# Optimization experiments

Hardware: AMD Instinct MI355X
Metric: run time of the kernel (lower is better)

The kernel has to match this reference:

```python
import jax, jax.numpy as jnp
import numpy as np

B, L, V, D, H, DK, NL, M = 4, 1024, 64, 256, 4, 64, 4, 20
FF = 4 * D
EPS = 1e-5


def _rel_table(seq_len, m):
    # abs(i-j), log-bucketed beyond m, clipped to [0, 2m] -> int indices [L, L]
    d = jnp.abs(jnp.arange(seq_len)[:, None] - jnp.arange(seq_len)[None, :]).astype(jnp.float32)
    d = jnp.where(d > m, m + jnp.log2(jnp.maximum(d - m, 1.0)), d)
    return jnp.clip(d, 0, 2 * m).astype(jnp.int32)


def _layer_norm(x, g, b):
    mu = jnp.mean(x, axis=-1, keepdims=True)
    var = jnp.mean(jnp.square(x - mu), axis=-1, keepdims=True)
    return (x - mu) * jax.lax.rsqrt(var + EPS) * g + b


def setup_inputs() -> dict:
    key = jax.random.key(0)
    ks = jax.random.split(key, 16)
    w = lambda i, shape: jax.random.normal(ks[i], shape, jnp.float32) * 0.05
    return {
        "x": jax.random.normal(ks[0], (B, L, V), jnp.float32),
        "emb": w(1, (V, D)),
        "Wq": w(2, (NL, D, H * DK)), "bq": jnp.zeros((NL, H * DK), jnp.float32),
        "Wk": w(3, (NL, D, H * DK)), "bk": jnp.zeros((NL, H * DK), jnp.float32),
        "Wv": w(4, (NL, D, H * DK)), "bv": jnp.zeros((NL, H * DK), jnp.float32),
        "Wo": w(5, (NL, H * DK, D)), "bo": jnp.zeros((NL, D), jnp.float32),
        "rel_k": 1.0 + w(6, (NL, 2 * M + 1, H)),  # multiplicative bias ~1
        "rel_b": w(7, (NL, 2 * M + 1, H)),
        "ln1_g": jnp.ones((NL, D), jnp.float32), "ln1_b": jnp.zeros((NL, D), jnp.float32),
        "W1": w(8, (NL, D, FF)), "b1": jnp.zeros((NL, FF), jnp.float32),
        "W2": w(9, (NL, FF, D)), "b2": jnp.zeros((NL, D), jnp.float32),
        "ln2_g": jnp.ones((NL, D), jnp.float32), "ln2_b": jnp.zeros((NL, D), jnp.float32),
    }


def reference(x, emb, Wq, bq, Wk, bk, Wv, bv, Wo, bo, rel_k, rel_b,
              ln1_g, ln1_b, W1, b1, W2, b2, ln2_g, ln2_b):
    h = x @ emb  # [B, L, D]  (dropout inactive: eval mode)
    table = _rel_table(L, M)  # [L, L] int32
    inv_sqrt_dk = jnp.float32(1.0 / np.sqrt(DK))
    attns = []
    for l in range(NL):
        q = (h @ Wq[l] + bq[l]).reshape(B, L, H, DK)
        k = (h @ Wk[l] + bk[l]).reshape(B, L, H, DK)
        v = (h @ Wv[l] + bv[l]).reshape(B, L, H, DK)
        scores = jnp.einsum('blhk,bmhk->bhlm', q, k) * inv_sqrt_dk
        # per-head relative-position bias (table symmetric, so axis order of L,L is immaterial)
        bias_k = jnp.transpose(rel_k[l][table], (2, 1, 0))  # [H, L, L]
        bias_b = jnp.transpose(rel_b[l][table], (2, 1, 0))  # [H, L, L]
        scores = scores * bias_k[None] + bias_b[None]
        attn = jax.nn.softmax(scores, axis=-1)  # attn dropout inactive (eval)
        attns.append(attn)
        out = jnp.einsum('bhlm,bmhk->blhk', attn, v).reshape(B, L, H * DK) @ Wo[l] + bo[l]
        # FeedForwardNetwork (note: source has NO residual connections)
        y = _layer_norm(out, ln1_g[l], ln1_b[l])
        y = jax.nn.gelu(y @ W1[l] + b1[l], approximate=False) @ W2[l] + b2[l]
        h = _layer_norm(y, ln2_g[l], ln2_b[l])
    avg_attn = jnp.mean(jnp.stack(attns, axis=0), axis=0)  # [B, H, L, L]
    return h.mean(axis=1), avg_attn
```

## Files before the change

### kernel.cpp

```cpp
#include <hip/hip_runtime.h>
#include <hip/hip_bf16.h>
#include <math.h>

#define Bn 4
#define Ln 1024
#define Vn 64
#define Dn 256
#define Hn 4
#define DKn 64
#define NLn 4
#define Mn 20
#define FFn 1024
#define NTOK (Bn * Ln)
#define QKVW 768
#define LOG2E 1.4426950408889634f
#define PELEMS (Bn * Hn * Ln * Ln)

typedef __attribute__((ext_vector_type(8))) short bf16x8;
typedef __attribute__((ext_vector_type(4))) float f32x4;

__device__ __forceinline__ ushort f2b(float f) {
    uint u = __float_as_uint(f);
    u += 0x7fff + ((u >> 16) & 1);
    return (ushort)(u >> 16);
}
__device__ __forceinline__ float b2f(ushort u) {
    return __uint_as_float(((uint)u) << 16);
}

__global__ __launch_bounds__(256) void embed_k(const float* __restrict__ X,
                                               const float* __restrict__ E,
                                               ushort* __restrict__ Hb) {
    __shared__ float xs[Vn];
    int n = blockIdx.x, d = threadIdx.x;
    if (threadIdx.x < Vn) xs[threadIdx.x] = X[n * Vn + threadIdx.x];
    __syncthreads();
    float s = 0.f;
#pragma unroll
    for (int v = 0; v < Vn; ++v) s += xs[v] * E[v * Dn + d];
    Hb[(size_t)n * Dn + d] = f2b(s);
}

__global__ __launch_bounds__(256) void relbias_k(const float* __restrict__ rk,
                                                 const float* __restrict__ rb,
                                                 float* __restrict__ bkT,
                                                 float* __restrict__ bbT) {
    int tid = blockIdx.x * 256 + threadIdx.x;
    int dist = tid & 1023;
    int hh = (tid >> 10) & 3;
    int l = tid >> 12;
    float dd = (float)dist;
    if (dist > Mn) dd = (float)Mn + log2f((float)(dist - Mn));
    if (dd > 2.0f * Mn) dd = 2.0f * Mn;
    int idx = (int)dd;
    bkT[tid] = rk[(l * (2 * Mn + 1) + idx) * Hn + hh] * 0.125f * LOG2E;
    bbT[tid] = rb[(l * (2 * Mn + 1) + idx) * Hn + hh] * LOG2E;
}

__global__ __launch_bounds__(256) void prep_bias(const float* __restrict__ bq,
                                                 const float* __restrict__ bk,
                                                 const float* __restrict__ bv,
                                                 float* __restrict__ bqkv) {
    int idx = blockIdx.x * 256 + threadIdx.x;
    int l = idx / QKVW, r = idx - l * QKVW;
    float v;
    if (r < 256)      v = bq[l * 256 + r];
    else if (r < 512) v = bk[l * 256 + r - 256];
    else              v = bv[l * 256 + r - 512];
    bqkv[idx] = v;
}

__global__ __launch_bounds__(256) void transpose_cvt(
    const float* __restrict__ src, ushort* __restrict__ dst,
    int R, int C, int srcLS, int dstLS) {
    __shared__ float s[32][33];
    src += (size_t)blockIdx.z * srcLS;
    dst += (size_t)blockIdx.z * dstLS;
    int r0 = blockIdx.y * 32, c0 = blockIdx.x * 32;
    int tx = threadIdx.x & 31, ty = threadIdx.x >> 5;
#pragma unroll
    for (int ii = 0; ii < 4; ++ii)
        s[ty + 8 * ii][tx] = src[(size_t)(r0 + ty + 8 * ii) * C + c0 + tx];
    __syncthreads();
#pragma unroll
    for (int ii = 0; ii < 4; ++ii)
        dst[(size_t)(c0 + ty + 8 * ii) * R + r0 + tx] = f2b(s[tx][ty + 8 * ii]);
}

#define GST 72
#define GEMM_KK_MFMA(KK)                                                      \
    {                                                                         \
        bf16x8 a0 = *(const bf16x8*)&As[(wm * 32 + l15) * GST + (KK)*32 + lg * 8];      \
        bf16x8 a1 = *(const bf16x8*)&As[(wm * 32 + 16 + l15) * GST + (KK)*32 + lg * 8]; \
        bf16x8 b0 = *(const bf16x8*)&Bs[(wn * 32 + l15) * GST + (KK)*32 + lg * 8];      \
        bf16x8 b1 = *(const bf16x8*)&Bs[(wn * 32 + 16 + l15) * GST + (KK)*32 + lg * 8]; \
        acc[0][0] = __builtin_amdgcn_mfma_f32_16x16x32_bf16(a0, b0, acc[0][0], 0, 0, 0); \
        acc[0][1] = __builtin_amdgcn_mfma_f32_16x16x32_bf16(a0, b1, acc[0][1], 0, 0, 0); \
        acc[1][0] = __builtin_amdgcn_mfma_f32_16x16x32_bf16(a1, b0, acc[1][0], 0, 0, 0); \
        acc[1][1] = __builtin_amdgcn_mfma_f32_16x16x32_bf16(a1, b1, acc[1][1], 0, 0, 0); \
    }

template <int LNA>
__global__ __launch_bounds__(256) void gemm_mfma(
    const ushort* __restrict__ A, const ushort* __restrict__ Bt,
    const float* __restrict__ bias, ushort* __restrict__ C,
    int M, int N, int K, int act,
    const float* __restrict__ lng, const float* __restrict__ lnb,
    ushort* __restrict__ Vt_out) {
    __shared__ __align__(16) ushort As[64 * GST];
    __shared__ __align__(16) ushort Bs[64 * GST];
    __shared__ float gl[256];
    __shared__ float bl[256];
    int t = threadIdx.x;
    int lane = t & 63, w = t >> 6;
    int wm = w >> 1, wn = w & 1;
    int l15 = lane & 15, lg = lane >> 4;
    int mBase = blockIdx.y * 64, nBase = blockIdx.x * 64;
    int lrow = t >> 2, lkc = (t & 3) * 16;
    const ushort* Ap = A + (size_t)(mBase + lrow) * K + lkc;
    const ushort* Bp = Bt + (size_t)(nBase + lrow) * K + lkc;
    f32x4 acc[2][2] = {};

    if constexpr (LNA) {
        uint4 areg[8];
        float s = 0.f;
#pragma unroll
        for (int kc = 0; kc < 4; ++kc)
#pragma unroll
            for (int h = 0; h < 2; ++h) {
                areg[kc * 2 + h] = *(const uint4*)(Ap + kc * 64 + h * 8);
                const ushort* e = (const ushort*)&areg[kc * 2 + h];
#pragma unroll
                for (int q = 0; q < 8; ++q) s += b2f(e[q]);
            }
        s += __shfl_xor(s, 1, 64);
        s += __shfl_xor(s, 2, 64);
        float mu = s * (1.0f / 256.0f);
        float vv = 0.f;
#pragma unroll
        for (int kc = 0; kc < 8; ++kc) {
            const ushort* e = (const ushort*)&areg[kc];
#pragma unroll
            for (int q = 0; q < 8; ++q) {
                float d = b2f(e[q]) - mu;
                vv += d * d;
            }
        }
        vv += __shfl_xor(vv, 1, 64);
        vv += __shfl_xor(vv, 2, 64);
        float rs = rsqrtf(vv * (1.0f / 256.0f) + 1e-5f);
        gl[t] = lng[t];
        bl[t] = lnb[t];
        __syncthreads();
#pragma unroll
        for (int kc = 0; kc < 4; ++kc) {
            uint4 bv0 = *(const uint4*)(Bp + kc * 64);
            uint4 bv1 = *(const uint4*)(Bp + kc * 64 + 8);
            __syncthreads();
#pragma unroll
            for (int h = 0; h < 2; ++h) {
                const ushort* e = (const ushort*)&areg[kc * 2 + h];
                ushort outv[8];
#pragma unroll
                for (int q = 0; q < 8; ++q) {
                    int col = kc * 64 + lkc + h * 8 + q;
                    outv[q] = f2b((b2f(e[q]) - mu) * rs * gl[col] + bl[col]);
                }
                *(uint4*)&As[lrow * GST + lkc + h * 8] = *(const uint4*)outv;
            }
            *(uint4*)&Bs[lrow * GST + lkc] = bv0;
            *(uint4*)&Bs[lrow * GST + lkc + 8] = bv1;
            __syncthreads();
            GEMM_KK_MFMA(0)
            GEMM_KK_MFMA(1)
        }
    } else {
        for (int k0 = 0; k0 < K; k0 += 64) {
            uint4 av0 = *(const uint4*)(Ap + k0);
            uint4 av1 = *(const uint4*)(Ap + k0 + 8);
            uint4 bv0 = *(const uint4*)(Bp + k0);
            uint4 bv1 = *(const uint4*)(Bp + k0 + 8);
            __syncthreads();
            *(uint4*)&As[lrow * GST + lkc] = av0;
            *(uint4*)&As[lrow * GST + lkc + 8] = av1;
            *(uint4*)&Bs[lrow * GST + lkc] = bv0;
            *(uint4*)&Bs[lrow * GST + lkc + 8] = bv1;
            __syncthreads();
            GEMM_KK_MFMA(0)
            GEMM_KK_MFMA(1)
        }
    }
    if (Vt_out != nullptr && nBase >= 512) {
#pragma unroll
        for (int ni = 0; ni < 2; ++ni) {
            int col = nBase + wn * 32 + ni * 16 + l15;
            float bc = bias[col];
            int d = col - 512;
#pragma unroll
            for (int mi = 0; mi < 2; ++mi) {
                int rb = mBase + wm * 32 + mi * 16 + lg * 4;
                int bb_ = rb >> 10, i_ = rb & 1023;
                size_t vb = ((size_t)(bb_ * 4 + (d >> 6)) * 64 + (d & 63)) * Ln + i_;
                ushort o4[4];
#pragma unroll
                for (int j = 0; j < 4; ++j) o4[j] = f2b(acc[mi][ni][j] + bc);
                *(ushort4*)&Vt_out[vb] = *(const ushort4*)o4;
            }
        }
        return;
    }
#pragma unroll
    for (int ni = 0; ni < 2; ++ni) {
        int col = nBase + wn * 32 + ni * 16 + l15;
        float bc = bias[col];
#pragma unroll
        for (int mi = 0; mi < 2; ++mi) {
            int rb = mBase + wm * 32 + mi * 16 + lg * 4;
#pragma unroll
            for (int j = 0; j < 4; ++j) {
                float v = acc[mi][ni][j] + bc;
                if (act) v = v * 0.5f * (1.0f + erff(v * 0.7071067811865475f));
                C[(size_t)(rb + j) * N + col] = f2b(v);
            }
        }
    }
}

#define PWST 40
#define NW 8
template <int MODE>
__global__ __launch_bounds__(512) void attn_fused(
    const ushort* __restrict__ qkv, const ushort* __restrict__ Vt,
    const float* __restrict__ bkTab, const float* __restrict__ bbTab,
    ushort* __restrict__ ctx, float* __restrict__ avg,
    ushort* __restrict__ Pout, int first) {
    __shared__ float bk_l[Ln];
    __shared__ float bb_l[Ln];
    __shared__ __align__(16) char uni[20480];
    __shared__ float mm[NW][16];
    __shared__ float ll[NW][16];

    int t = threadIdx.x;
    int lane = t & 63, w = t >> 6;
    int wn = w & 3, wc = w >> 2;
    int l15 = lane & 15, lg = lane >> 4;

    ushort* pwh = (ushort*)&uni[w * 2560];
    ushort* pwl = (ushort*)&uni[w * 2560 + 1280];

    int bid = blockIdx.x;
    int xcd = bid & 7, sub = bid >> 3;
    int bh = xcd * 2 + (sub >> 6);
    int q = sub & 63;
    int b = bh >> 2, hh = bh & 3;
    int i0 = q * 16;

#pragma unroll
    for (int ii = 0; ii < 2; ++ii) {
        bk_l[t + 512 * ii] = bkTab[hh * Ln + t + 512 * ii];
        bb_l[t + 512 * ii] = bbTab[hh * Ln + t + 512 * ii];
    }
    __syncthreads();

    bf16x8 qa0, qa1;
    {
        const ushort* qp = qkv + (size_t)(b * Ln + i0 + l15) * QKVW + hh * DKn;
        qa0 = *(const bf16x8*)(qp + lg * 8);
        qa1 = *(const bf16x8*)(qp + 32 + lg * 8);
    }

    const ushort* kbase = qkv + (size_t)(b * Ln) * QKVW + Dn + hh * DKn;

    f32x4 sv[8];
    float m[4] = {-1e30f, -1e30f, -1e30f, -1e30f};
#pragma unroll
    for (int cl = 0; cl < 8; ++cl) {
        int c = wc * 8 + cl;
        const ushort* kp = kbase + (size_t)(c * 64 + wn * 16 + l15) * QKVW;
        bf16x8 k0 = *(const bf16x8*)(kp + lg * 8);
        bf16x8 k1 = *(const bf16x8*)(kp + 32 + lg * 8);
        f32x4 acc = {};
        acc = __builtin_amdgcn_mfma_f32_16x16x32_bf16(qa0, k0, acc, 0, 0, 0);
        acc = __builtin_amdgcn_mfma_f32_16x16x32_bf16(qa1, k1, acc, 0, 0, 0);
        int j = c * 64 + wn * 16 + l15;
#pragma unroll
        for (int r = 0; r < 4; ++r) {
            int i = i0 + lg * 4 + r;
            int dist = (i > j) ? (i - j) : (j - i);
            float s = acc[r] * bk_l[dist] + bb_l[dist];
            sv[cl][r] = s;
            m[r] = fmaxf(m[r], s);
        }
    }
#pragma unroll
    for (int mask = 1; mask < 16; mask <<= 1)
#pragma unroll
        for (int r = 0; r < 4; ++r) m[r] = fmaxf(m[r], __shfl_xor(m[r], mask, 64));
    if (l15 == 0)
#pragma unroll
        for (int r = 0; r < 4; ++r) mm[w][lg * 4 + r] = m[r];
    __syncthreads();
#pragma unroll
    for (int r = 0; r < 4; ++r) {
        int row = lg * 4 + r;
        float m0 = fmaxf(fmaxf(mm[0][row], mm[1][row]), fmaxf(mm[2][row], mm[3][row]));
        float m1 = fmaxf(fmaxf(mm[4][row], mm[5][row]), fmaxf(mm[6][row], mm[7][row]));
        m[r] = fmaxf(m0, m1);
    }
    float lsum[4] = {0.f, 0.f, 0.f, 0.f};
#pragma unroll
    for (int cl = 0; cl < 8; ++cl)
#pragma unroll
        for (int r = 0; r < 4; ++r) {
            float p = exp2f(sv[cl][r] - m[r]);
            sv[cl][r] = p;
            lsum[r] += p;
        }
#pragma unroll
    for (int mask = 1; mask < 16; mask <<= 1)
#pragma unroll
        for (int r = 0; r < 4; ++r) lsum[r] += __shfl_xor(lsum[r], mask, 64);
    if (l15 == 0)
#pragma unroll
        for (int r = 0; r < 4; ++r) ll[w][lg * 4 + r] = lsum[r];
    __syncthreads();
    float invl[4];
#pragma unroll
    for (int r = 0; r < 4; ++r) {
        int row = lg * 4 + r;
        invl[r] = 1.0f / (ll[0][row] + ll[1][row] + ll[2][row] + ll[3][row] +
                          ll[4][row] + ll[5][row] + ll[6][row] + ll[7][row]);
    }

    const ushort* vbase = Vt + (size_t)bh * DKn * Ln;
    float* avgrow = avg + ((size_t)bh * Ln + i0) * Ln;
    int iw = lane >> 2, jq = lane & 3;
    f32x4 acco[4] = {};
#pragma unroll
    for (int p = 0; p < 4; ++p) {
        const int c0 = wc * 8 + 2 * p, c1 = c0 + 1;
        float aold[2][4];
        if (MODE == 0 && !first) {
#pragma unroll
            for (int cc = 0; cc < 2; ++cc)
#pragma unroll
                for (int r = 0; r < 4; ++r)
                    aold[cc][r] = avgrow[(size_t)(lg * 4 + r) * Ln +
                                         (c0 + cc) * 64 + wn * 16 + l15];
        }
#pragma unroll
        for (int cc = 0; cc < 2; ++cc)
#pragma unroll
            for (int r = 0; r < 4; ++r) {
                float pv = sv[2 * p + cc][r] * invl[r];
                sv[2 * p + cc][r] = pv;
                ushort ph = f2b(pv);
                int off = (lg * 4 + r) * PWST + cc * 16 + l15;
                pwh[off] = ph;
                pwl[off] = f2b(pv - b2f(ph));
            }
        int kcol = (lg < 2 ? c0 : c1) * 64 + wn * 16 + (lg & 1) * 8;
        bf16x8 va0 = *(const bf16x8*)(vbase + (size_t)(0 * 16 + l15) * Ln + kcol);
        bf16x8 va1 = *(const bf16x8*)(vbase + (size_t)(1 * 16 + l15) * Ln + kcol);
        bf16x8 va2 = *(const bf16x8*)(vbase + (size_t)(2 * 16 + l15) * Ln + kcol);
        bf16x8 va3 = *(const bf16x8*)(vbase + (size_t)(3 * 16 + l15) * Ln + kcol);
        bf16x8 pbh = *(const bf16x8*)&pwh[l15 * PWST + lg * 8];
        bf16x8 pbl = *(const bf16x8*)&pwl[l15 * PWST + lg * 8];
        acco[0] = __builtin_amdgcn_mfma_f32_16x16x32_bf16(va0, pbh, acco[0], 0, 0, 0);
        acco[1] = __builtin_amdgcn_mfma_f32_16x16x32_bf16(va1, pbh, acco[1], 0, 0, 0);
        acco[2] = __builtin_amdgcn_mfma_f32_16x16x32_bf16(va2, pbh, acco[2], 0, 0, 0);
        acco[3] = __builtin_amdgcn_mfma_f32_16x16x32_bf16(va3, pbh, acco[3], 0, 0, 0);
        acco[0] = __builtin_amdgcn_mfma_f32_16x16x32_bf16(va0, pbl, acco[0], 0, 0, 0);
        acco[1] = __builtin_amdgcn_mfma_f32_16x16x32_bf16(va1, pbl, acco[1], 0, 0, 0);
        acco[2] = __builtin_amdgcn_mfma_f32_16x16x32_bf16(va2, pbl, acco[2], 0, 0, 0);
        acco[3] = __builtin_amdgcn_mfma_f32_16x16x32_bf16(va3, pbl, acco[3], 0, 0, 0);
        if (MODE == 0) {
#pragma unroll
            for (int cc = 0; cc < 2; ++cc)
#pragma unroll
                for (int r = 0; r < 4; ++r) {
                    float v = 0.25f * sv[2 * p + cc][r];
                    if (!first) v += aold[cc][r];
                    avgrow[(size_t)(lg * 4 + r) * Ln + (c0 + cc) * 64 + wn * 16 + l15] = v;
                }
        } else if (MODE == 1) {
            size_t tb = ((((size_t)bid * 8 + w) * 4 + p) * 2) * 256 + (size_t)lane * 4;
            ushort4 ph0 = *(const ushort4*)&pwh[iw * PWST + 0 * 16 + jq * 4];
            ushort4 ph1 = *(const ushort4*)&pwh[iw * PWST + 1 * 16 + jq * 4];
            *(ushort4*)&Pout[tb] = ph0;
            *(ushort4*)&Pout[tb + 256] = ph1;
        } else {
#pragma unroll
            for (int cc = 0; cc < 2; ++cc) {
                int c = c0 + cc;
                size_t tb = ((((size_t)bid * 8 + w) * 4 + p) * 2 + cc) * 256 +
                            (size_t)lane * 4;
                ushort4 p0 = *(const ushort4*)&Pout[tb];
                ushort4 p1 = *(const ushort4*)&Pout[(size_t)PELEMS + tb];
                ushort4 p2 = *(const ushort4*)&Pout[(size_t)2 * PELEMS + tb];
                ushort4 p3 = *(const ushort4*)&pwh[iw * PWST + cc * 16 + jq * 4];
                const ushort* q0 = (const ushort*)&p0;
                const ushort* q1 = (const ushort*)&p1;
                const ushort* q2 = (const ushort*)&p2;
                const ushort* q3 = (const ushort*)&p3;
                size_t base = ((size_t)(bh * Ln) + i0 + iw) * Ln +
                              c * 64 + wn * 16 + jq * 4;
                float4 o;
                float* op_ = (float*)&o;
#pragma unroll
                for (int k = 0; k < 4; ++k)
                    op_[k] = 0.25f * (b2f(q0[k]) + b2f(q1[k]) + b2f(q2[k]) + b2f(q3[k]));
                *(float4*)&avg[base] = o;
            }
        }
    }

    __syncthreads();
    {
        float* op = (float*)&uni[wn * 4096];
        if (wc == 1) {
#pragma unroll
            for (int dg = 0; dg < 4; ++dg)
#pragma unroll
                for (int r = 0; r < 4; ++r)
                    op[(dg * 16 + lg * 4 + r) * 16 + l15] = acco[dg][r];
        }
    }
    __syncthreads();
    {
        float* op = (float*)&uni[wn * 4096];
        if (wc == 0) {
#pragma unroll
            for (int dg = 0; dg < 4; ++dg)
#pragma unroll
                for (int r = 0; r < 4; ++r)
                    op[(dg * 16 + lg * 4 + r) * 16 + l15] += acco[dg][r];
        }
    }
    __syncthreads();
#pragma unroll
    for (int k = 0; k < 2; ++k) {
        int idx = t + 512 * k;
        float v = ((const float*)&uni[0])[idx] + ((const float*)&uni[4096])[idx] +
                  ((const float*)&uni[8192])[idx] + ((const float*)&uni[12288])[idx];
        int dd = idx >> 4, ii = idx & 15;
        ctx[(size_t)(b * Ln + i0 + ii) * Dn + hh * DKn + dd] = f2b(v);
    }
}

__global__ __launch_bounds__(256) void layernorm_k(const ushort* __restrict__ X,
                                                   const float* __restrict__ g,
                                                   const float* __restrict__ bta,
                                                   ushort* __restrict__ Y) {
    int w = threadIdx.x >> 6, lane = threadIdx.x & 63;
    int row = blockIdx.x * 4 + w;
    const ushort* xr = X + (size_t)row * Dn;
    float x[4];
#pragma unroll
    for (int ii = 0; ii < 4; ++ii) x[ii] = b2f(xr[lane + 64 * ii]);
    float s = x[0] + x[1] + x[2] + x[3];
#pragma unroll
    for (int m = 1; m < 64; m <<= 1) s += __shfl_xor(s, m, 64);
    float mu = s * (1.0f / 256.0f);
    float vs = 0.f;
#pragma unroll
    for (int ii = 0; ii < 4; ++ii) {
        float d = x[ii] - mu;
        vs += d * d;
    }
#pragma unroll
    for (int m = 1; m < 64; m <<= 1) vs += __shfl_xor(vs, m, 64);
    float rs = rsqrtf(vs * (1.0f / 256.0f) + 1e-5f);
#pragma unroll
    for (int ii = 0; ii < 4; ++ii) {
        int d = lane + 64 * ii;
        Y[(size_t)row * Dn + d] = f2b((x[ii] - mu) * rs * g[d] + bta[d]);
    }
}

__global__ __launch_bounds__(256) void mean_part_k(const ushort* __restrict__ Hb,
                                                   float* __restrict__ part) {
    int blk = blockIdx.x;
    int b = blk >> 4, g = blk & 15;
    int d = threadIdx.x;
    float s = 0.f;
#pragma unroll
    for (int r = 0; r < 64; ++r)
        s += b2f(Hb[(size_t)(b * Ln + g * 64 + r) * Dn + d]);
    part[(size_t)blk * Dn + d] = s;
}
__global__ __launch_bounds__(256) void mean_final_k(const float* __restrict__ part,
                                                    float* __restrict__ out) {
    int b = blockIdx.x, d = threadIdx.x;
    float s = 0.f;
#pragma unroll
    for (int g = 0; g < 16; ++g) s += part[(size_t)(b * 16 + g) * Dn + d];
    out[b * Dn + d] = s * (1.0f / (float)Ln);
}

extern "C" void kernel_launch(void* const* d_in, const int* in_sizes, int n_in,
                              void* d_out, int out_size, void* d_ws, size_t ws_size,
                              hipStream_t stream) {
    const float* x    = (const float*)d_in[0];
    const float* emb  = (const float*)d_in[1];
    const float* Wq   = (const float*)d_in[2];
    const float* bq   = (const float*)d_in[3];
    const float* Wk   = (const float*)d_in[4];
    const float* bk   = (const float*)d_in[5];
    const float* Wv   = (const float*)d_in[6];
    const float* bv   = (const float*)d_in[7];
    const float* Wo   = (const float*)d_in[8];
    const float* bo   = (const float*)d_in[9];
    const float* rk   = (const float*)d_in[10];
    const float* rb   = (const float*)d_in[11];
    const float* ln1g = (const float*)d_in[12];
    const float* ln1b = (const float*)d_in[13];
    const float* W1   = (const float*)d_in[14];
    const float* b1   = (const float*)d_in[15];
    const float* W2   = (const float*)d_in[16];
    const float* b2   = (const float*)d_in[17];
    const float* ln2g = (const float*)d_in[18];
    const float* ln2b = (const float*)d_in[19];

    float* out = (float*)d_out;
    float* avg = out + Bn * Dn;

    char* ws = (char*)d_ws;
    const size_t MB = 1024 * 1024;
    ushort* hb   = (ushort*)(ws);
    ushort* qkvb = (ushort*)(ws + 2 * MB);
    ushort* ctxb = (ushort*)(ws + 8 * MB);
    ushort* t1   = (ushort*)(ws + 10 * MB);
    ushort* ffb  = (ushort*)(ws + 12 * MB);
    ushort* qkvT = (ushort*)(ws + 20 * MB);
    ushort* WoT  = (ushort*)(ws + 22 * MB);
    ushort* W1T  = (ushort*)(ws + 23 * MB);
    ushort* W2T  = (ushort*)(ws + 25 * MB);
    float*  bqkv = (float*)(ws + 27 * MB);
    float*  bkT  = (float*)(ws + 27 * MB + 65536);
    float*  bbT  = (float*)(ws + 27 * MB + 131072);
    ushort* Vt   = (ushort*)(ws + 30 * MB);
    float*  mpart= (float*)(ws + 33 * MB);
    ushort* Pbuf = (ushort*)(ws + 36 * MB);

    const size_t need = 36 * MB + (size_t)3 * PELEMS * sizeof(ushort);
    const bool fancy = (ws_size >= need);

    embed_k<<<NTOK, 256, 0, stream>>>(x, emb, hb);
    relbias_k<<<64, 256, 0, stream>>>(rk, rb, bkT, bbT);
    prep_bias<<<12, 256, 0, stream>>>(bq, bk, bv, bqkv);

    dim3 t88(8, 8, NLn);
    transpose_cvt<<<t88, 256, 0, stream>>>(Wq, qkvT + 0,      256, 256, 65536, 196608);
    transpose_cvt<<<t88, 256, 0, stream>>>(Wk, qkvT + 65536,  256, 256, 65536, 196608);
    transpose_cvt<<<t88, 256, 0, stream>>>(Wv, qkvT + 131072, 256, 256, 65536, 196608);
    transpose_cvt<<<t88, 256, 0, stream>>>(Wo, WoT,           256, 256, 65536, 65536);
    transpose_cvt<<<dim3(32, 8, NLn), 256, 0, stream>>>(W1, W1T, 256, 1024, 262144, 262144);
    transpose_cvt<<<dim3(8, 32, NLn), 256, 0, stream>>>(W2, W2T, 1024, 256, 262144, 262144);

    for (int l = 0; l < NLn; ++l) {
        if (l == 0) {
            gemm_mfma<0><<<dim3(12, 64), 256, 0, stream>>>(
                hb, qkvT + (size_t)l * 196608, bqkv + l * QKVW, qkvb,
                NTOK, QKVW, Dn, 0, nullptr, nullptr, Vt);
        } else {
            gemm_mfma<1><<<dim3(12, 64), 256, 0, stream>>>(
                hb, qkvT + (size_t)l * 196608, bqkv + l * QKVW, qkvb,
                NTOK, QKVW, Dn, 0, ln2g + (l - 1) * 256, ln2b + (l - 1) * 256, Vt);
        }
        if (fancy) {
            if (l < 3) {
                attn_fused<1><<<1024, 512, 0, stream>>>(
                    qkvb, Vt, bkT + l * Hn * Ln, bbT + l * Hn * Ln, ctxb, avg,
                    Pbuf + (size_t)l * PELEMS, 0);
            } else {
                attn_fused<2><<<1024, 512, 0, stream>>>(
                    qkvb, Vt, bkT + l * Hn * Ln, bbT + l * Hn * Ln, ctxb, avg,
                    Pbuf, 0);
            }
        } else {
            attn_fused<0><<<1024, 512, 0, stream>>>(
                qkvb, Vt, bkT + l * Hn * Ln, bbT + l * Hn * Ln, ctxb, avg,
                (ushort*)Pbuf, (l == 0) ? 1 : 0);
        }
        gemm_mfma<0><<<dim3(4, 64), 256, 0, stream>>>(
            ctxb, WoT + (size_t)l * 65536, bo + l * 256, t1,
            NTOK, Dn, Dn, 0, nullptr, nullptr, nullptr);
        gemm_mfma<1><<<dim3(16, 64), 256, 0, stream>>>(
            t1, W1T + (size_t)l * 262144, b1 + l * FFn, ffb,
            NTOK, FFn, Dn, 1, ln1g + l * 256, ln1b + l * 256, nullptr);
        gemm_mfma<0><<<dim3(4, 64), 256, 0, stream>>>(
            ffb, W2T + (size_t)l * 262144, b2 + l * 256, hb,
            NTOK, Dn, FFn, 0, nullptr, nullptr, nullptr);
    }
    layernorm_k<<<NTOK / 4, 256, 0, stream>>>(
        hb, ln2g + 3 * 256, ln2b + 3 * 256, hb);
    mean_part_k<<<64, 256, 0, stream>>>(hb, mpart);
    mean_final_k<<<Bn, 256, 0, stream>>>(mpart, out);
}
```

Baseline: 375.5 us.

## Add 128x128-tile MFMA GEMM with fused LayerNorm and split-K FFN down-projection

```diff
diff --git a/kernel.cpp b/kernel.cpp
--- a/kernel.cpp
+++ b/kernel.cpp
@@ -224,6 +224,177 @@
             }
         }
     }
+}
+
+#define G2ST 72
+template <int LNA, int SPLITK>
+__global__ __launch_bounds__(256) void gemm128(
+    const ushort* __restrict__ A, const ushort* __restrict__ Bt,
+    const float* __restrict__ bias, ushort* __restrict__ C,
+    float* __restrict__ Cpart,
+    int M, int N, int K, int act,
+    const float* __restrict__ lng, const float* __restrict__ lnb,
+    ushort* __restrict__ Vt_out) {
+    __shared__ __align__(16) ushort As[128 * G2ST];
+    __shared__ __align__(16) ushort Bs[128 * G2ST];
+    __shared__ float gl[256];
+    __shared__ float bl[256];
+    int t = threadIdx.x;
+    int lane = t & 63, w = t >> 6;
+    int wm = w >> 1, wn = w & 1;
+    int l15 = lane & 15, lg = lane >> 4;
+    int mBase = blockIdx.y * 128, nBase = blockIdx.x * 128;
+    int srow = t >> 1, skof = (t & 1) * 32;
+    int kchunk = (SPLITK > 1) ? (K / SPLITK) : K;
+    int kbeg = (SPLITK > 1) ? blockIdx.z * kchunk : 0;
+    const ushort* Ap = A + (size_t)(mBase + srow) * K + kbeg + skof;
+    const ushort* Bp = Bt + (size_t)(nBase + srow) * K + kbeg + skof;
+    f32x4 acc[4][4] = {};
+
+    float mu = 0.f, rs = 0.f;
+    uint4 areg[16];
+    if constexpr (LNA) {
+        float s = 0.f;
+#pragma unroll
+        for (int kc = 0; kc < 4; ++kc)
+#pragma unroll
+            for (int q = 0; q < 4; ++q) {
+                areg[kc * 4 + q] = *(const uint4*)(Ap + kc * 64 + q * 8);
+                const ushort* e = (const ushort*)&areg[kc * 4 + q];
+#pragma unroll
+                for (int z = 0; z < 8; ++z) s += b2f(e[z]);
+            }
+        s += __shfl_xor(s, 1, 64);
+        mu = s * (1.0f / 256.0f);
+        float vv = 0.f;
+#pragma unroll
+        for (int q = 0; q < 16; ++q) {
+            const ushort* e = (const ushort*)&areg[q];
+#pragma unroll
+            for (int z = 0; z < 8; ++z) {
+                float d = b2f(e[z]) - mu;
+                vv += d * d;
+            }
+        }
+        vv += __shfl_xor(vv, 1, 64);
+        rs = rsqrtf(vv * (1.0f / 256.0f) + 1e-5f);
+        gl[t] = lng[t];
+        bl[t] = lnb[t];
+    }
+
+#pragma unroll 1
+    for (int kc = 0; kc < kchunk / 64; ++kc) {
+        uint4 av[4], bv[4];
+        if constexpr (!LNA) {
+#pragma unroll
+            for (int q = 0; q < 4; ++q) av[q] = *(const uint4*)(Ap + kc * 64 + q * 8);
+        }
+#pragma unroll
+        for (int q = 0; q < 4; ++q) bv[q] = *(const uint4*)(Bp + kc * 64 + q * 8);
+        __syncthreads();
+        if constexpr (LNA) {
+#pragma unroll
+            for (int q = 0; q < 4; ++q) {
+                const ushort* e = (const ushort*)&areg[kc * 4 + q];
+                ushort outv[8];
+#pragma unroll
+                for (int z = 0; z < 8; ++z) {
+                    int col = kc * 64 + skof + q * 8 + z;
+                    outv[z] = f2b((b2f(e[z]) - mu) * rs * gl[col] + bl[col]);
+                }
+                *(uint4*)&As[srow * G2ST + skof + q * 8] = *(const uint4*)outv;
+            }
+        } else {
+#pragma unroll
+            for (int q = 0; q < 4; ++q)
+                *(uint4*)&As[srow * G2ST + skof + q * 8] = av[q];
+        }
+#pragma unroll
+        for (int q = 0; q < 4; ++q)
+            *(uint4*)&Bs[srow * G2ST + skof + q * 8] = bv[q];
+        __syncthreads();
+#pragma unroll
+        for (int kk = 0; kk < 2; ++kk) {
+            bf16x8 af[4], bf[4];
+#pragma unroll
+            for (int mi = 0; mi < 4; ++mi)
+                af[mi] = *(const bf16x8*)&As[(wm * 64 + mi * 16 + l15) * G2ST + kk * 32 + lg * 8];
+#pragma unroll
+            for (int ni = 0; ni < 4; ++ni)
+                bf[ni] = *(const bf16x8*)&Bs[(wn * 64 + ni * 16 + l15) * G2ST + kk * 32 + lg * 8];
+#pragma unroll
+            for (int mi = 0; mi < 4; ++mi)
+#pragma unroll
+                for (int ni = 0; ni < 4; ++ni)
+                    acc[mi][ni] = __builtin_amdgcn_mfma_f32_16x16x32_bf16(
+                        af[mi], bf[ni], acc[mi][ni], 0, 0, 0);
+        }
+    }
+
+    if (Vt_out != nullptr && nBase >= 512) {
+#pragma unroll
+        for (int ni = 0; ni < 4; ++ni) {
+            int col = nBase + wn * 64 + ni * 16 + l15;
+            float bc = bias[col];
+            int d = col - 512;
+#pragma unroll
+            for (int mi = 0; mi < 4; ++mi) {
+                int rb = mBase + wm * 64 + mi * 16 + lg * 4;
+                int bb_ = rb >> 10, i_ = rb & 1023;
+                size_t vb = ((size_t)(bb_ * 4 + (d >> 6)) * 64 + (d & 63)) * Ln + i_;
+                ushort o4[4];
+#pragma unroll
+                for (int j = 0; j < 4; ++j) o4[j] = f2b(acc[mi][ni][j] + bc);
+                *(ushort4*)&Vt_out[vb] = *(const ushort4*)o4;
+            }
+        }
+        return;
+    }
+    if constexpr (SPLITK > 1) {
+#pragma unroll
+        for (int ni = 0; ni < 4; ++ni) {
+            int col = nBase + wn * 64 + ni * 16 + l15;
+#pragma unroll
+            for (int mi = 0; mi < 4; ++mi) {
+                int rb = mBase + wm * 64 + mi * 16 + lg * 4;
+#pragma unroll
+                for (int j = 0; j < 4; ++j)
+                    Cpart[((size_t)blockIdx.z * M + rb + j) * N + col] = acc[mi][ni][j];
+            }
+        }
+        return;
+    }
+#pragma unroll
+    for (int ni = 0; ni < 4; ++ni) {
+        int col = nBase + wn * 64 + ni * 16 + l15;
+        float bc = bias[col];
+#pragma unroll
+        for (int mi = 0; mi < 4; ++mi) {
+            int rb = mBase + wm * 64 + mi * 16 + lg * 4;
+#pragma unroll
+            for (int j = 0; j < 4; ++j) {
+                float v = acc[mi][ni][j] + bc;
+                if (act) v = v * 0.5f * (1.0f + erff(v * 0.7071067811865475f));
+                C[(size_t)(rb + j) * N + col] = f2b(v);
+            }
+        }
+    }
+}
+
+__global__ __launch_bounds__(256) void combine_k(const float* __restrict__ part,
+                                                 const float* __restrict__ bias,
+                                                 ushort* __restrict__ C) {
+    size_t e = ((size_t)blockIdx.x * 256 + threadIdx.x) * 4;
+    const size_t MN = (size_t)NTOK * Dn;
+    float4 s = *(const float4*)&bias[(int)(e & 255)];
+#pragma unroll
+    for (int z = 0; z < 4; ++z) {
+        float4 p = *(const float4*)&part[z * MN + e];
+        s.x += p.x; s.y += p.y; s.z += p.z; s.w += p.w;
+    }
+    ushort4 o;
+    o.x = f2b(s.x); o.y = f2b(s.y); o.z = f2b(s.z); o.w = f2b(s.w);
+    *(ushort4*)&C[e] = o;
 }
 
 #define PWST 40
@@ -542,8 +713,9 @@
     ushort* Vt   = (ushort*)(ws + 30 * MB);
     float*  mpart= (float*)(ws + 33 * MB);
     ushort* Pbuf = (ushort*)(ws + 36 * MB);
-
-    const size_t need = 36 * MB + (size_t)3 * PELEMS * sizeof(ushort);
+    float*  fpart= (float*)(ws + 132 * MB);
+
+    const size_t need = 132 * MB + (size_t)4 * NTOK * Dn * sizeof(float);
     const bool fancy = (ws_size >= need);
 
     embed_k<<<NTOK, 256, 0, stream>>>(x, emb, hb);
@@ -559,16 +731,16 @@
     transpose_cvt<<<dim3(8, 32, NLn), 256, 0, stream>>>(W2, W2T, 1024, 256, 262144, 262144);
 
     for (int l = 0; l < NLn; ++l) {
-        if (l == 0) {
-            gemm_mfma<0><<<dim3(12, 64), 256, 0, stream>>>(
-                hb, qkvT + (size_t)l * 196608, bqkv + l * QKVW, qkvb,
-                NTOK, QKVW, Dn, 0, nullptr, nullptr, Vt);
-        } else {
-            gemm_mfma<1><<<dim3(12, 64), 256, 0, stream>>>(
-                hb, qkvT + (size_t)l * 196608, bqkv + l * QKVW, qkvb,
-                NTOK, QKVW, Dn, 0, ln2g + (l - 1) * 256, ln2b + (l - 1) * 256, Vt);
-        }
         if (fancy) {
+            if (l == 0) {
+                gemm128<0, 1><<<dim3(6, 32), 256, 0, stream>>>(
+                    hb, qkvT + (size_t)l * 196608, bqkv + l * QKVW, qkvb, nullptr,
+                    NTOK, QKVW, Dn, 0, nullptr, nullptr, Vt);
+            } else {
+                gemm128<1, 1><<<dim3(6, 32), 256, 0, stream>>>(
+                    hb, qkvT + (size_t)l * 196608, bqkv + l * QKVW, qkvb, nullptr,
+                    NTOK, QKVW, Dn, 0, ln2g + (l - 1) * 256, ln2b + (l - 1) * 256, Vt);
+            }
             if (l < 3) {
                 attn_fused<1><<<1024, 512, 0, stream>>>(
                     qkvb, Vt, bkT + l * Hn * Ln, bbT + l * Hn * Ln, ctxb, avg,
@@ -578,20 +750,39 @@
                     qkvb, Vt, bkT + l * Hn * Ln, bbT + l * Hn * Ln, ctxb, avg,
                     Pbuf, 0);
             }
+            gemm_mfma<0><<<dim3(4, 64), 256, 0, stream>>>(
+                ctxb, WoT + (size_t)l * 65536, bo + l * 256, t1,
+                NTOK, Dn, Dn, 0, nullptr, nullptr, nullptr);
+            gemm128<1, 1><<<dim3(8, 32), 256, 0, stream>>>(
+                t1, W1T + (size_t)l * 262144, b1 + l * FFn, ffb, nullptr,
+                NTOK, FFn, Dn, 1, ln1g + l * 256, ln1b + l * 256, nullptr);
+            gemm128<0, 4><<<dim3(2, 32, 4), 256, 0, stream>>>(
+                ffb, W2T + (size_t)l * 262144, nullptr, nullptr, fpart,
+                NTOK, Dn, FFn, 0, nullptr, nullptr, nullptr);
+            combine_k<<<1024, 256, 0, stream>>>(fpart, b2 + l * 256, hb);
         } else {
+            if (l == 0) {
+                gemm_mfma<0><<<dim3(12, 64), 256, 0, stream>>>(
+                    hb, qkvT + (size_t)l * 196608, bqkv + l * QKVW, qkvb,
+                    NTOK, QKVW, Dn, 0, nullptr, nullptr, Vt);
+            } else {
+                gemm_mfma<1><<<dim3(12, 64), 256, 0, stream>>>(
+                    hb, qkvT + (size_t)l * 196608, bqkv + l * QKVW, qkvb,
+                    NTOK, QKVW, Dn, 0, ln2g + (l - 1) * 256, ln2b + (l - 1) * 256, Vt);
+            }
             attn_fused<0><<<1024, 512, 0, stream>>>(
                 qkvb, Vt, bkT + l * Hn * Ln, bbT + l * Hn * Ln, ctxb, avg,
                 (ushort*)Pbuf, (l == 0) ? 1 : 0);
-        }
-        gemm_mfma<0><<<dim3(4, 64), 256, 0, stream>>>(
-            ctxb, WoT + (size_t)l * 65536, bo + l * 256, t1,
-            NTOK, Dn, Dn, 0, nullptr, nullptr, nullptr);
-        gemm_mfma<1><<<dim3(16, 64), 256, 0, stream>>>(
-            t1, W1T + (size_t)l * 262144, b1 + l * FFn, ffb,
-            NTOK, FFn, Dn, 1, ln1g + l * 256, ln1b + l * 256, nullptr);
-        gemm_mfma<0><<<dim3(4, 64), 256, 0, stream>>>(
-            ffb, W2T + (size_t)l * 262144, b2 + l * 256, hb,
-            NTOK, Dn, FFn, 0, nullptr, nullptr, nullptr);
+            gemm_mfma<0><<<dim3(4, 64), 256, 0, stream>>>(
+                ctxb, WoT + (size_t)l * 65536, bo + l * 256, t1,
+                NTOK, Dn, Dn, 0, nullptr, nullptr, nullptr);
+            gemm_mfma<1><<<dim3(16, 64), 256, 0, stream>>>(
+                t1, W1T + (size_t)l * 262144, b1 + l * FFn, ffb,
+                NTOK, FFn, Dn, 1, ln1g + l * 256, ln1b + l * 256, nullptr);
+            gemm_mfma<0><<<dim3(4, 64), 256, 0, stream>>>(
+                ffb, W2T + (size_t)l * 262144, b2 + l * 256, hb,
+                NTOK, Dn, FFn, 0, nullptr, nullptr, nullptr);
+        }
     }
     layernorm_k<<<NTOK / 4, 256, 0, stream>>>(
         hb, ln2g + 3 * 256, ln2b + 3 * 256, hb);
```

After: 567.9 us. 1.51x slower.
